# Kernel tuning notes

Hardware: AMD Instinct MI355X
Metric: run time of the kernel (lower is better)

## Reference

```python
import jax, jax.numpy as jnp
import numpy as np
import math

D = 2048  # hidden_size
B, S = 4, 2048
EPS = 1e-5


def _ln(z, g, b):
    m = jnp.mean(z, axis=-1, keepdims=True)
    v = jnp.mean(jnp.square(z - m), axis=-1, keepdims=True)
    return (z - m) * jax.lax.rsqrt(v + EPS) * g + b


def _rotate_half(x):
    h = x.shape[-1] // 2
    return jnp.concatenate([-x[..., h:], x[..., :h]], axis=-1)


def _mas_normalize(logits):
    m = jnp.max(jnp.abs(logits), axis=-1, keepdims=True)
    return logits / (m + 1e-9)


def setup_inputs() -> dict:
    key = jax.random.key(0)
    ks = jax.random.split(key, 12)
    std = 0.02
    return {
        "x": jax.random.normal(ks[0], (B, S, D), dtype=jnp.float32),
        "position_ids": jnp.arange(S, dtype=jnp.int32),
        "ln1_g": jnp.ones((D,), jnp.float32),
        "ln1_b": jnp.zeros((D,), jnp.float32),
        # stacked params for [q, k, v, o]
        "mu_w": std * jax.random.normal(ks[1], (4, D, D), dtype=jnp.float32),
        "mu_b": jnp.zeros((4, D), jnp.float32),
        "proto_w": std * jax.random.normal(ks[2], (4, D, D), dtype=jnp.float32),
        "gate": jnp.zeros((4, D), jnp.float32),
        "pt_w": std * jax.random.normal(ks[3], (4, D, D), dtype=jnp.float32),
        "pln_g": jnp.ones((4, D), jnp.float32),
        "pln_b": jnp.zeros((4, D), jnp.float32),
        "incoming": std * jax.random.normal(ks[4], (4, D, D), dtype=jnp.float32),
    }


def reference(x, position_ids, ln1_g, ln1_b, mu_w, mu_b, proto_w, gate,
              pt_w, pln_g, pln_b, incoming):
    d = x.shape[-1]
    inv_sqrt_d = 1.0 / math.sqrt(d)

    # proto_state = proto_weight + LN(Linear(incoming))  per module [4, D, D]
    prc = jnp.einsum('nij,noj->nio', incoming, pt_w)
    proto_state = proto_w + _ln(prc, pln_g[:, None, :], pln_b[:, None, :])

    ln1_out = _ln(x, ln1_g, ln1_b)            # [B,S,D]
    ctx = jnp.mean(ln1_out, axis=1)           # [B,D]

    # qkv computation outputs: silu(ln1_out @ mu_w.T + mu_b) for n in {q,k,v}
    comp = jax.nn.silu(jnp.einsum('bsd,nod->nbso', ln1_out, mu_w[:3])
                       + mu_b[:3][:, None, None, :])            # [3,B,S,D]
    # routing from context vector
    match_ctx = jnp.einsum('bd,nod->nbo', ctx, proto_state[:3]) * inv_sqrt_d
    routing = match_ctx + gate[:3][:, None, :]                  # [3,B,D]
    gating = _mas_normalize(routing)
    masked = gating[:, :, None, :] * comp                       # [3,B,S,D]
    q, k, v = masked[0], masked[1], masked[2]

    # RoPE over full hidden dim (num_heads == 1)
    seq = position_ids.shape[0]
    inv_freq = 1.0 / (10000.0 ** (jnp.arange(0, d, 2, dtype=jnp.float32) / d))
    t = jnp.arange(seq, dtype=jnp.float32)
    freqs = t[:, None] * inv_freq[None, :]
    emb = jnp.concatenate([freqs, freqs], axis=-1)              # [S,D]
    cos = jnp.cos(emb)[position_ids]
    sin = jnp.sin(emb)[position_ids]
    q = q * cos + _rotate_half(q) * sin
    k = k * cos + _rotate_half(k) * sin

    # causal single-head attention, scale 1/sqrt(head_dim=D)
    scores = jnp.einsum('bqd,bkd->bqk', q, k) * inv_sqrt_d      # [B,S,S]
    causal = jnp.tril(jnp.ones((seq, seq), dtype=bool))
    scores = jnp.where(causal, scores, jnp.finfo(scores.dtype).min)
    probs = jax.nn.softmax(scores, axis=-1)
    attn_out = jnp.einsum('bqk,bkd->bqd', probs, v)             # [B,S,D]

    # output SPL + routing
    ctx_o = jnp.mean(attn_out, axis=1)
    c_o = jax.nn.silu(jnp.einsum('bsd,od->bso', attn_out, mu_w[3]) + mu_b[3])
    match_o = jnp.einsum('bd,od->bo', ctx_o, proto_state[3]) * inv_sqrt_d
    gating_o = _mas_normalize(match_o + gate[3])
    x_out = x + gating_o[:, None, :] * c_o
    return x_out
```

## Files before the change

kernel.cpp:

```cpp
#include <hip/hip_runtime.h>
#include <hip/hip_bf16.h>
#include <hip/hip_fp16.h>

#define Dh 2048
#define Bh 4
#define Sh 2048
#define NROW 8192
#define HALF 1024
#define INV_SQRT_D 0.022097086912079608f
#define LNEPS 1e-5f

typedef __hip_bfloat16 bf16;
typedef short short8 __attribute__((ext_vector_type(8)));
typedef float f32x4 __attribute__((ext_vector_type(4)));
typedef unsigned short ushort8v __attribute__((ext_vector_type(8)));
typedef unsigned short ushort4v __attribute__((ext_vector_type(4)));

__device__ inline float h2f_bits(unsigned short u) {
  __half h;
  *(unsigned short*)&h = u;
  return __half2float(h);
}

__device__ inline float warp_sum(float x) {
#pragma unroll
  for (int o = 32; o > 0; o >>= 1) x += __shfl_down(x, o);
  return x;
}
__device__ inline float warp_max(float x) {
#pragma unroll
  for (int o = 32; o > 0; o >>= 1) x = fmaxf(x, __shfl_down(x, o));
  return x;
}
__device__ inline float block_sum(float x, float* sm4) {
  x = warp_sum(x);
  int w = threadIdx.x >> 6;
  if ((threadIdx.x & 63) == 0) sm4[w] = x;
  __syncthreads();
  float r = sm4[0] + sm4[1] + sm4[2] + sm4[3];
  __syncthreads();
  return r;
}
__device__ inline float block_max(float x, float* sm4) {
  x = warp_max(x);
  int w = threadIdx.x >> 6;
  if ((threadIdx.x & 63) == 0) sm4[w] = x;
  __syncthreads();
  float r = fmaxf(fmaxf(sm4[0], sm4[1]), fmaxf(sm4[2], sm4[3]));
  __syncthreads();
  return r;
}

__device__ inline void gload_lds16(const void* g, void* lds) {
  __builtin_amdgcn_global_load_lds(
      (const __attribute__((address_space(1))) unsigned int*)(unsigned long long)g,
      (__attribute__((address_space(3))) unsigned int*)(unsigned long long)lds,
      16, 0, 0);
}

#define MM4(R, AF, B0, B1, B2, B3)                                             \
  acc[R][0] = __builtin_amdgcn_mfma_f32_16x16x32_bf16(AF, B0, acc[R][0], 0, 0, 0); \
  acc[R][1] = __builtin_amdgcn_mfma_f32_16x16x32_bf16(AF, B1, acc[R][1], 0, 0, 0); \
  acc[R][2] = __builtin_amdgcn_mfma_f32_16x16x32_bf16(AF, B2, acc[R][2], 0, 0, 0); \
  acc[R][3] = __builtin_amdgcn_mfma_f32_16x16x32_bf16(AF, B3, acc[R][3], 0, 0, 0);

template <int MODE>
__global__ __launch_bounds__(512) void pgemm(
    const bf16* __restrict__ Aall, const bf16* __restrict__ Ball,
    void* __restrict__ Call, int N, int K, int lda, int ldb,
    long sAz, long sBz, long sCz,
    const float* __restrict__ e0, const float* __restrict__ e1,
    const float* __restrict__ e2) {
  const int bm0 = blockIdx.x * 256;
  const int bn0 = blockIdx.y * 256;
  if (MODE == 2 && bn0 > bm0 + 255) return;
  const int z = blockIdx.z;
  const bf16* A = Aall + (long)z * sAz;
  const bf16* B = Ball + (long)z * sBz;

  __shared__ __align__(16) char smem[131072];
  const int tid = threadIdx.x;
  const int l = tid & 63, w = tid >> 6;
  const int wr = w >> 2, wc = w & 3;

  f32x4 acc[8][4] = {};
  const int nt = K >> 6;

  const int sg = (((l & 7) ^ ((l >> 3) & 7)) << 3);
  const int srow = (w << 3) + (l >> 3);
  const bf16* aS0 = A + (long)(bm0 + srow) * lda + sg;
  const bf16* aS1 = A + (long)(bm0 + 64 + srow) * lda + sg;
  const bf16* aS2 = A + (long)(bm0 + 128 + srow) * lda + sg;
  const bf16* aS3 = A + (long)(bm0 + 192 + srow) * lda + sg;
  const bf16* bT0 = B + (long)(bn0 + srow) * ldb + sg;
  const bf16* bT1 = B + (long)(bn0 + 64 + srow) * ldb + sg;
  const bf16* bT2 = B + (long)(bn0 + 128 + srow) * ldb + sg;
  const bf16* bT3 = B + (long)(bn0 + 192 + srow) * ldb + sg;
  char* const dA = smem + (w << 10);
  char* const dB = smem + 65536 + (w << 10);

  auto stageA = [&](int tt) {
    int boff = (tt & 1) << 15;
    gload_lds16(aS0 + (tt << 6), dA + boff);
    gload_lds16(aS1 + (tt << 6), dA + boff + 8192);
    gload_lds16(aS2 + (tt << 6), dA + boff + 16384);
    gload_lds16(aS3 + (tt << 6), dA + boff + 24576);
  };
  auto stageB = [&](int tt) {
    int boff = (tt & 1) << 15;
    gload_lds16(bT0 + (tt << 6), dB + boff);
    gload_lds16(bT1 + (tt << 6), dB + boff + 8192);
    gload_lds16(bT2 + (tt << 6), dB + boff + 16384);
    gload_lds16(bT3 + (tt << 6), dB + boff + 24576);
  };

  stageA(0); stageB(0);
  if (nt > 1) stageB(1);
  if (nt > 1) asm volatile("s_waitcnt vmcnt(4)" ::: "memory");
  else        asm volatile("s_waitcnt vmcnt(0)" ::: "memory");
  __builtin_amdgcn_sched_barrier(0);
  asm volatile("s_barrier" ::: "memory");

  const int rslot = (((l >> 4) ^ (l & 7)) << 4);
  const int abyte = (((wr << 7) + (l & 15)) << 7) + rslot;
  const int bbyte = (((wc << 6) + (l & 15)) << 7) + rslot;

  for (int t = 0; t < nt; ++t) {
    const char* Ab = smem + ((t & 1) << 15);
    const char* Bb = smem + 65536 + ((t & 1) << 15);
    short8 b00 = *(const short8*)(Bb + bbyte);
    short8 b01 = *(const short8*)(Bb + bbyte + 2048);
    short8 b02 = *(const short8*)(Bb + bbyte + 4096);
    short8 b03 = *(const short8*)(Bb + bbyte + 6144);
    short8 b10 = *(const short8*)(Bb + (bbyte ^ 64));
    short8 b11 = *(const short8*)(Bb + ((bbyte + 2048) ^ 64));
    short8 b12 = *(const short8*)(Bb + ((bbyte + 4096) ^ 64));
    short8 b13 = *(const short8*)(Bb + ((bbyte + 6144) ^ 64));
    short8 a0 = *(const short8*)(Ab + abyte);
    short8 a1 = *(const short8*)(Ab + abyte + 2048);
    short8 a2 = *(const short8*)(Ab + abyte + 4096);
    short8 a3 = *(const short8*)(Ab + abyte + 6144);
    short8 a4 = *(const short8*)(Ab + abyte + 8192);
    short8 a5 = *(const short8*)(Ab + abyte + 10240);
    short8 a6 = *(const short8*)(Ab + abyte + 12288);
    short8 a7 = *(const short8*)(Ab + abyte + 14336);
    if (t + 1 < nt) stageA(t + 1);
    MM4(0, a0, b00, b01, b02, b03) MM4(1, a1, b00, b01, b02, b03)
    MM4(2, a2, b00, b01, b02, b03) MM4(3, a3, b00, b01, b02, b03)
    MM4(4, a4, b00, b01, b02, b03) MM4(5, a5, b00, b01, b02, b03)
    MM4(6, a6, b00, b01, b02, b03) MM4(7, a7, b00, b01, b02, b03)
    asm volatile("s_waitcnt lgkmcnt(0)" ::: "memory");
    asm volatile("s_barrier" ::: "memory");
    short8 c0 = *(const short8*)(Ab + (abyte ^ 64));
    short8 c1 = *(const short8*)(Ab + ((abyte + 2048) ^ 64));
    short8 c2 = *(const short8*)(Ab + ((abyte + 4096) ^ 64));
    short8 c3 = *(const short8*)(Ab + ((abyte + 6144) ^ 64));
    short8 c4 = *(const short8*)(Ab + ((abyte + 8192) ^ 64));
    short8 c5 = *(const short8*)(Ab + ((abyte + 10240) ^ 64));
    short8 c6 = *(const short8*)(Ab + ((abyte + 12288) ^ 64));
    short8 c7 = *(const short8*)(Ab + ((abyte + 14336) ^ 64));
    if (t + 2 < nt) stageB(t + 2);
    MM4(0, c0, b10, b11, b12, b13) MM4(1, c1, b10, b11, b12, b13)
    MM4(2, c2, b10, b11, b12, b13) MM4(3, c3, b10, b11, b12, b13)
    MM4(4, c4, b10, b11, b12, b13) MM4(5, c5, b10, b11, b12, b13)
    MM4(6, c6, b10, b11, b12, b13) MM4(7, c7, b10, b11, b12, b13)
    if (t < nt - 1) {
      asm volatile("s_waitcnt lgkmcnt(0)" ::: "memory");
      if (t + 2 < nt) asm volatile("s_waitcnt vmcnt(4)" ::: "memory");
      else            asm volatile("s_waitcnt vmcnt(0)" ::: "memory");
      __builtin_amdgcn_sched_barrier(0);
      asm volatile("s_barrier" ::: "memory");
    }
  }

  const int lc = l & 15, lr4 = (l >> 4) << 2;
#pragma unroll
  for (int fr = 0; fr < 8; ++fr) {
    int gr0 = bm0 + (wr << 7) + fr * 16 + lr4;
#pragma unroll
    for (int fc = 0; fc < 4; ++fc) {
      int gc = bn0 + (wc << 6) + fc * 16 + lc;
#pragma unroll
      for (int qv = 0; qv < 4; ++qv) {
        int gr = gr0 + qv;
        float a = acc[fr][fc][qv];
        if (MODE == 0) {
          ((float*)Call + (long)z * sCz)[(long)gr * N + gc] = a;
        } else if (MODE == 1) {
          float val = a + e0[z * Dh + gc];
          float sil = val / (1.f + __expf(-val));
          int bb = gr >> 11;
          float g = e1[(z * Bh + bb) * Dh + gc];
          ((bf16*)Call + (long)z * sCz)[(long)gr * N + gc] =
              __float2bfloat16(sil * g);
        } else if (MODE == 2) {
          ((__half*)Call + (long)z * sCz)[(long)gr * N + gc] =
              __float2half(a * INV_SQRT_D);
        } else {
          float val = a + e0[gc];
          float sil = val / (1.f + __expf(-val));
          int bb = gr >> 11;
          ((float*)Call)[(long)gr * N + gc] =
              e2[(long)gr * N + gc] + e1[bb * Dh + gc] * sil;
        }
      }
    }
  }
}

#define MM(R, AF)                                                              \
  acc[R][0] = __builtin_amdgcn_mfma_f32_16x16x32_bf16(AF, b0, acc[R][0], 0, 0, 0); \
  acc[R][1] = __builtin_amdgcn_mfma_f32_16x16x32_bf16(AF, b1, acc[R][1], 0, 0, 0); \
  acc[R][2] = __builtin_amdgcn_mfma_f32_16x16x32_bf16(AF, b2, acc[R][2], 0, 0, 0); \
  acc[R][3] = __builtin_amdgcn_mfma_f32_16x16x32_bf16(AF, b3, acc[R][3], 0, 0, 0);

__global__ __launch_bounds__(512) void pgemm_h(
    const bf16* __restrict__ Aall, const bf16* __restrict__ Ball,
    bf16* __restrict__ Call, int N, int lda, int ldb,
    long sAz, long sBz, long sCz) {
  const int fid = blockIdx.x;
  const int p = fid >> 8, q = fid & 255;
  const int mh = q >> 5;
  const int z = (q >> 3) & 3, ni = q & 7;
  const int mi = p ? (15 - mh) : mh;
  const int bm0 = mi * 128, bn0 = ni * 256;
  const bf16* A = Aall + (long)z * sAz;
  const bf16* B = Ball + (long)z * sBz;

  __shared__ __align__(16) char smem[49152];
  const int tid = threadIdx.x;
  const int l = tid & 63, w = tid >> 6;
  const int wr = w >> 2, wc = w & 3;
  f32x4 acc[4][4] = {};
  const int nt = (bm0 + 128) >> 5;

  const int sg = (((l & 3) ^ ((l >> 3) & 3)) << 3);
  const int srow = (w << 4) + (l >> 2);
  const bf16* aS  = A + (long)(bm0 + srow) * lda + sg;
  const bf16* bS0 = B + (long)(bn0 + srow) * ldb + sg;
  const bf16* bS1 = B + (long)(bn0 + 128 + srow) * ldb + sg;
  char* const dA = smem + (w << 10);
  char* const dB = smem + 8192 + (w << 10);

  auto stageA = [&](int tt) {
    gload_lds16(aS + (tt << 5), dA + (tt & 1) * 24576);
  };
  auto stageB = [&](int tt) {
    int boff = (tt & 1) * 24576;
    gload_lds16(bS0 + (tt << 5), dB + boff);
    gload_lds16(bS1 + (tt << 5), dB + boff + 8192);
  };

  stageA(0); stageB(0);
  if (nt > 1) stageB(1);
  if (nt > 1) asm volatile("s_waitcnt vmcnt(2)" ::: "memory");
  else        asm volatile("s_waitcnt vmcnt(0)" ::: "memory");
  __builtin_amdgcn_sched_barrier(0);
  asm volatile("s_barrier" ::: "memory");

  const int rslot = (((l >> 4) ^ ((l >> 1) & 3)) << 4);
  const int abyte = (((wr << 6) + (l & 15)) << 6) + rslot;
  const int bbyte = (((wc << 6) + (l & 15)) << 6) + rslot;

  for (int t = 0; t < nt; ++t) {
    const char* Ab = smem + (t & 1) * 24576;
    const char* Bb = Ab + 8192;
    short8 b0 = *(const short8*)(Bb + bbyte);
    short8 b1 = *(const short8*)(Bb + bbyte + 1024);
    short8 b2 = *(const short8*)(Bb + bbyte + 2048);
    short8 b3 = *(const short8*)(Bb + bbyte + 3072);
    short8 a0 = *(const short8*)(Ab + abyte);
    short8 a1 = *(const short8*)(Ab + abyte + 1024);
    if (t + 1 < nt) stageA(t + 1);
    MM(0, a0) MM(1, a1)
    asm volatile("s_waitcnt lgkmcnt(0)" ::: "memory");
    asm volatile("s_barrier" ::: "memory");
    short8 a2 = *(const short8*)(Ab + abyte + 2048);
    short8 a3 = *(const short8*)(Ab + abyte + 3072);
    if (t + 2 < nt) stageB(t + 2);
    MM(2, a2) MM(3, a3)
    if (t < nt - 1) {
      asm volatile("s_waitcnt lgkmcnt(0)" ::: "memory");
      if (t + 2 < nt) asm volatile("s_waitcnt vmcnt(2)" ::: "memory");
      else            asm volatile("s_waitcnt vmcnt(0)" ::: "memory");
      __builtin_amdgcn_sched_barrier(0);
      asm volatile("s_barrier" ::: "memory");
    }
  }

  const int lc = l & 15, lr4 = (l >> 4) << 2;
  bf16* C = Call + (long)z * sCz;
#pragma unroll
  for (int fr = 0; fr < 4; ++fr) {
    int gr0 = bm0 + (wr << 6) + fr * 16 + lr4;
#pragma unroll
    for (int fc = 0; fc < 4; ++fc) {
      int gc = bn0 + (wc << 6) + fc * 16 + lc;
#pragma unroll
      for (int qv = 0; qv < 4; ++qv)
        C[(long)(gr0 + qv) * N + gc] = __float2bfloat16(acc[fr][fc][qv]);
    }
  }
}

__global__ __launch_bounds__(256) void cvt3_kernel(
    const float* __restrict__ s0, const float* __restrict__ s1,
    const float* __restrict__ s2, bf16* __restrict__ o0, bf16* __restrict__ o1,
    bf16* __restrict__ o2, long n) {
  const float* in = (blockIdx.y == 0) ? s0 : (blockIdx.y == 1) ? s1 : s2;
  bf16* out = (blockIdx.y == 0) ? o0 : (blockIdx.y == 1) ? o1 : o2;
  long i = ((long)blockIdx.x * 256 + threadIdx.x) * 4;
  if (i >= n) return;
  float4 v = *(const float4*)(in + i);
  out[i + 0] = __float2bfloat16(v.x);
  out[i + 1] = __float2bfloat16(v.y);
  out[i + 2] = __float2bfloat16(v.z);
  out[i + 3] = __float2bfloat16(v.w);
}

__global__ __launch_bounds__(256) void transpose_kernel(const bf16* __restrict__ in,
                                                        bf16* __restrict__ out) {
  __shared__ bf16 t[64][65];
  int b = blockIdx.z;
  int s0 = blockIdx.x * 64, d0 = blockIdx.y * 64;
  const bf16* ib = in + (long)b * Sh * Dh;
  bf16* ob = out + (long)b * Sh * Dh;
  int tx = threadIdx.x & 63, ty = threadIdx.x >> 6;
#pragma unroll
  for (int r = ty; r < 64; r += 4) t[r][tx] = ib[(long)(s0 + r) * Dh + d0 + tx];
  __syncthreads();
#pragma unroll
  for (int r = ty; r < 64; r += 4) ob[(long)(d0 + r) * Sh + s0 + tx] = t[tx][r];
}

__global__ __launch_bounds__(256) void ln1_kernel(const float* __restrict__ x,
    const float* __restrict__ g, const float* __restrict__ b, bf16* __restrict__ out) {
  __shared__ float sm4[4];
  long r = blockIdx.x;
  const float* row = x + r * Dh;
  int i0 = threadIdx.x * 4, i1 = 1024 + threadIdx.x * 4;
  float4 v0 = *(const float4*)(row + i0);
  float4 v1 = *(const float4*)(row + i1);
  float s = v0.x + v0.y + v0.z + v0.w + v1.x + v1.y + v1.z + v1.w;
  float s2 = v0.x * v0.x + v0.y * v0.y + v0.z * v0.z + v0.w * v0.w +
             v1.x * v1.x + v1.y * v1.y + v1.z * v1.z + v1.w * v1.w;
  s = block_sum(s, sm4);
  s2 = block_sum(s2, sm4);
  float mean = s * (1.f / Dh);
  float rstd = rsqrtf(s2 * (1.f / Dh) - mean * mean + LNEPS);
  float4 g0 = *(const float4*)(g + i0);
  float4 g1 = *(const float4*)(g + i1);
  float4 b0 = *(const float4*)(b + i0);
  float4 b1 = *(const float4*)(b + i1);
  ushort4v u0, u1;
  {
    bf16 t0 = __float2bfloat16((v0.x - mean) * rstd * g0.x + b0.x);
    bf16 t1 = __float2bfloat16((v0.y - mean) * rstd * g0.y + b0.y);
    bf16 t2 = __float2bfloat16((v0.z - mean) * rstd * g0.z + b0.z);
    bf16 t3 = __float2bfloat16((v0.w - mean) * rstd * g0.w + b0.w);
    u0[0] = *(unsigned short*)&t0; u0[1] = *(unsigned short*)&t1;
    u0[2] = *(unsigned short*)&t2; u0[3] = *(unsigned short*)&t3;
    bf16 s0b = __float2bfloat16((v1.x - mean) * rstd * g1.x + b1.x);
    bf16 s1b = __float2bfloat16((v1.y - mean) * rstd * g1.y + b1.y);
    bf16 s2b = __float2bfloat16((v1.z - mean) * rstd * g1.z + b1.z);
    bf16 s3b = __float2bfloat16((v1.w - mean) * rstd * g1.w + b1.w);
    u1[0] = *(unsigned short*)&s0b; u1[1] = *(unsigned short*)&s1b;
    u1[2] = *(unsigned short*)&s2b; u1[3] = *(unsigned short*)&s3b;
  }
  *(ushort4v*)(out + r * Dh + i0) = u0;
  *(ushort4v*)(out + r * Dh + i1) = u1;
}

__global__ __launch_bounds__(256) void meanrow_kernel(const bf16* __restrict__ in,
                                                      float* __restrict__ outbd) {
  int gid = blockIdx.x * 256 + threadIdx.x;
  int s0 = blockIdx.y * 128;
  long base = ((long)(gid >> 11) * Sh + s0) * Dh + (gid & 2047);
  float s = 0.f;
  for (int t = 0; t < 128; ++t) s += __bfloat162float(in[base + (long)t * Dh]);
  atomicAdd(&outbd[gid], s * (1.f / Sh));
}

__global__ __launch_bounds__(256) void route_kernel(
    const float* __restrict__ prc, const float* __restrict__ proto_w,
    const float* __restrict__ pln_g, const float* __restrict__ pln_b,
    const float* __restrict__ gate, const float* __restrict__ ctx,
    float* __restrict__ routing, float* __restrict__ ps3) {
  __shared__ float sm4[4];
  int i = blockIdx.x, n = blockIdx.y;
  long rb = ((long)n * Dh + i) * Dh;
  float v[8];
  float s = 0.f, s2 = 0.f;
#pragma unroll
  for (int c = 0; c < 8; ++c) {
    float t = prc[rb + threadIdx.x + c * 256];
    v[c] = t; s += t; s2 += t * t;
  }
  s = block_sum(s, sm4);
  s2 = block_sum(s2, sm4);
  float mean = s * (1.f / Dh);
  float rstd = rsqrtf(s2 * (1.f / Dh) - mean * mean + LNEPS);
  if (n == 3) {
#pragma unroll
    for (int c = 0; c < 8; ++c) {
      int o = threadIdx.x + c * 256;
      float ps = proto_w[rb + o] + (v[c] - mean) * rstd * pln_g[3 * Dh + o] + pln_b[3 * Dh + o];
      ps3[(long)i * Dh + o] = ps;
    }
  } else {
    float acc[4] = {0.f, 0.f, 0.f, 0.f};
#pragma unroll
    for (int c = 0; c < 8; ++c) {
      int o = threadIdx.x + c * 256;
      float ps = proto_w[rb + o] + (v[c] - mean) * rstd * pln_g[n * Dh + o] + pln_b[n * Dh + o];
#pragma unroll
      for (int b = 0; b < 4; ++b) acc[b] += ps * ctx[b * Dh + o];
    }
    for (int b = 0; b < 4; ++b) {
      float r = block_sum(acc[b], sm4);
      if (threadIdx.x == 0)
        routing[(n * 4 + b) * Dh + i] = r * INV_SQRT_D + gate[n * Dh + i];
    }
  }
}

__global__ __launch_bounds__(256) void route_o_kernel(
    const float* __restrict__ ps3, const float* __restrict__ ctxo,
    const float* __restrict__ gate, float* __restrict__ routing) {
  __shared__ float sm4[4];
  int i = blockIdx.x;
  float acc[4] = {0.f, 0.f, 0.f, 0.f};
#pragma unroll
  for (int c = 0; c < 8; ++c) {
    int o = threadIdx.x + c * 256;
    float p = ps3[(long)i * Dh + o];
#pragma unroll
    for (int b = 0; b < 4; ++b) acc[b] += p * ctxo[b * Dh + o];
  }
  for (int b = 0; b < 4; ++b) {
    float r = block_sum(acc[b], sm4);
    if (threadIdx.x == 0)
      routing[(12 + b) * Dh + i] = r * INV_SQRT_D + gate[3 * Dh + i];
  }
}

__global__ __launch_bounds__(256) void masnorm_kernel(const float* __restrict__ rin,
                                                      float* __restrict__ gout) {
  __shared__ float sm4[4];
  long r = blockIdx.x;
  float m = 0.f;
#pragma unroll
  for (int c = 0; c < 8; ++c)
    m = fmaxf(m, fabsf(rin[r * Dh + threadIdx.x + c * 256]));
  m = block_max(m, sm4);
  float inv = 1.f / (m + 1e-9f);
#pragma unroll
  for (int c = 0; c < 8; ++c) {
    int o = threadIdx.x + c * 256;
    gout[r * Dh + o] = rin[r * Dh + o] * inv;
  }
}

__global__ __launch_bounds__(256) void rope_table_kernel(float* __restrict__ cosT,
                                                         float* __restrict__ sinT) {
  int idx = blockIdx.x * 256 + threadIdx.x;
  int t = idx >> 10, f = idx & 1023;
  float inv_freq = expf(-(float)f * (9.210340371976184f / 1024.f));
  float ang = (float)t * inv_freq;
  cosT[idx] = cosf(ang);
  sinT[idx] = sinf(ang);
}

__global__ __launch_bounds__(256) void rope_kernel(bf16* __restrict__ q, bf16* __restrict__ k,
    const int* __restrict__ pos, const float* __restrict__ cosT,
    const float* __restrict__ sinT) {
  long r = blockIdx.x;
  int s = (int)(r & (Sh - 1));
  int p = pos[s];
#pragma unroll
  for (int c = 0; c < 4; ++c) {
    int t = threadIdx.x + c * 256;
    float cv = cosT[(long)p * HALF + t];
    float sv = sinT[(long)p * HALF + t];
    long i1 = r * Dh + t, i2 = i1 + HALF;
    float q1 = __bfloat162float(q[i1]), q2 = __bfloat162float(q[i2]);
    q[i1] = __float2bfloat16(q1 * cv - q2 * sv);
    q[i2] = __float2bfloat16(q2 * cv + q1 * sv);
    float k1 = __bfloat162float(k[i1]), k2 = __bfloat162float(k[i2]);
    k[i1] = __float2bfloat16(k1 * cv - k2 * sv);
    k[i2] = __float2bfloat16(k2 * cv + k1 * sv);
  }
}

__global__ __launch_bounds__(256) void softmax_kernel(const unsigned short* __restrict__ scores,
                                                      bf16* __restrict__ probs) {
  __shared__ float buf[Sh];
  __shared__ float sm4[4];
  long r = blockIdx.x;
  int qi = (int)(r & (Sh - 1));
  const unsigned short* row = scores + r * (long)Sh;
  bf16* prow = probs + r * (long)Sh;
  int tid = threadIdx.x;
  int n = qi + 1, nv = n & ~7;
  float m = -3.0e38f;
  for (int o = tid * 8; o < nv; o += 2048) {
    ushort8v v = *(const ushort8v*)(row + o);
#pragma unroll
    for (int j = 0; j < 8; ++j) {
      float x = h2f_bits(v[j]);
      buf[o + j] = x;
      m = fmaxf(m, x);
    }
  }
  for (int o = nv + tid; o < n; o += 256) {
    float x = h2f_bits(row[o]); buf[o] = x; m = fmaxf(m, x);
  }
  m = block_max(m, sm4);
  float s = 0.f;
  for (int o = tid; o < n; o += 256) {
    float e = __expf(buf[o] - m); buf[o] = e; s += e;
  }
  s = block_sum(s, sm4);
  float inv = 1.f / s;
  for (int o = tid * 8; o < nv; o += 2048) {
    ushort8v u;
#pragma unroll
    for (int j = 0; j < 8; ++j) {
      bf16 t = __float2bfloat16(buf[o + j] * inv);
      u[j] = *(unsigned short*)&t;
    }
    *(ushort8v*)(prow + o) = u;
  }
  for (int o = nv + tid; o < n; o += 256) prow[o] = __float2bfloat16(buf[o] * inv);
  int za = (n + 7) & ~7;
  for (int o = n + tid; o < za && o < Sh; o += 256) prow[o] = __float2bfloat16(0.f);
  ushort8v zz = {0, 0, 0, 0, 0, 0, 0, 0};
  for (int o = za + tid * 8; o < Sh; o += 2048) *(ushort8v*)(prow + o) = zz;
}

extern "C" void kernel_launch(void* const* d_in, const int* in_sizes, int n_in,
                              void* d_out, int out_size, void* d_ws, size_t ws_size,
                              hipStream_t stream) {
  const float* x       = (const float*)d_in[0];
  const int*   pos     = (const int*)d_in[1];
  const float* ln1_g   = (const float*)d_in[2];
  const float* ln1_b   = (const float*)d_in[3];
  const float* mu_w    = (const float*)d_in[4];
  const float* mu_b    = (const float*)d_in[5];
  const float* proto_w = (const float*)d_in[6];
  const float* gate    = (const float*)d_in[7];
  const float* pt_w    = (const float*)d_in[8];
  const float* pln_g   = (const float*)d_in[9];
  const float* pln_b   = (const float*)d_in[10];
  const float* incoming= (const float*)d_in[11];

  char* w = (char*)d_ws;
  const long BF = 33554432L;
  bf16*  ln1    = (bf16*)(w);
  bf16*  qb     = (bf16*)(w + BF);
  bf16*  kb     = (bf16*)(w + 2 * BF);
  bf16*  vb     = (bf16*)(w + 3 * BF);
  bf16*  attn   = (bf16*)(w + 4 * BF);
  bf16*  mu_wb  = (bf16*)(w + 5 * BF);
  bf16*  ptw_b  = (bf16*)(w + 6 * BF);
  bf16*  vT     = ptw_b;
  bf16*  inc_b  = (bf16*)(w + 7 * BF);
  bf16*  probs  = inc_b;
  float* ps3    = (float*)(w + 8 * BF);
  float* cosT   = (float*)(w + 8 * BF + 16777216L);
  float* sinT   = cosT + (long)Sh * HALF;
  float* ctx    = sinT + (long)Sh * HALF;
  float* ctxo   = ctx + Bh * Dh;
  float* routing= ctxo + Bh * Dh;
  float* gating = routing + 16 * Dh;
  float*  prc    = (float*)d_out;
  __half* scores = (__half*)d_out;

  const long DD4 = 4L * Dh * Dh;

  hipMemsetAsync(ctx, 0, 2L * Bh * Dh * sizeof(float), stream);

  rope_table_kernel<<<(Sh * HALF) / 256, 256, 0, stream>>>(cosT, sinT);
  cvt3_kernel<<<dim3(DD4 / 1024, 3), 256, 0, stream>>>(
      mu_w, incoming, pt_w, mu_wb, inc_b, ptw_b, DD4);
  ln1_kernel<<<NROW, 256, 0, stream>>>(x, ln1_g, ln1_b, ln1);
  meanrow_kernel<<<dim3(32, 16), 256, 0, stream>>>(ln1, ctx);
  pgemm<0><<<dim3(8, 8, 4), 512, 0, stream>>>(
      inc_b, ptw_b, prc, Dh, Dh, Dh, Dh,
      (long)Dh * Dh, (long)Dh * Dh, (long)Dh * Dh, nullptr, nullptr, nullptr);
  route_kernel<<<dim3(Dh, 4), 256, 0, stream>>>(prc, proto_w, pln_g, pln_b,
                                                gate, ctx, routing, ps3);
  masnorm_kernel<<<12, 256, 0, stream>>>(routing, gating);
  pgemm<1><<<dim3(32, 8, 3), 512, 0, stream>>>(
      ln1, mu_wb, qb, Dh, Dh, Dh, Dh,
      0L, (long)Dh * Dh, (long)NROW * Dh, mu_b, gating, nullptr);
  rope_kernel<<<NROW, 256, 0, stream>>>(qb, kb, pos, cosT, sinT);
  pgemm<2><<<dim3(8, 8, 4), 512, 0, stream>>>(
      qb, kb, scores, Sh, Dh, Dh, Dh,
      (long)Sh * Dh, (long)Sh * Dh, (long)Sh * Sh, nullptr, nullptr, nullptr);
  softmax_kernel<<<Bh * Sh, 256, 0, stream>>>((const unsigned short*)scores, probs);
  transpose_kernel<<<dim3(32, 32, 4), 256, 0, stream>>>(vb, vT);
  pgemm_h<<<512, 512, 0, stream>>>(
      probs, vT, attn, Dh, Sh, Sh,
      (long)Sh * Sh, (long)Dh * Sh, (long)Sh * Dh);
  meanrow_kernel<<<dim3(32, 16), 256, 0, stream>>>(attn, ctxo);
  route_o_kernel<<<Dh, 256, 0, stream>>>(ps3, ctxo, gate, routing);
  masnorm_kernel<<<4, 256, 0, stream>>>(routing + 12 * Dh, gating + 12 * Dh);
  pgemm<4><<<dim3(32, 8, 1), 512, 0, stream>>>(
      attn, mu_wb + 3L * Dh * Dh, d_out, Dh, Dh, Dh, Dh,
      0L, 0L, 0L, mu_b + 3 * Dh, gating + 12 * Dh, x);
}
```

Measured before the change: 630.9 us.

## Switch GEMM to 32x32x16 MFMA with a fragment-native LDS layout

Replaces the 16x16x32 bf16 MFMA tiling with 32x32x16 instructions, so each wave holds a 4x2 grid of 32x32 accumulators. The global-to-LDS staging is rearranged so each wave writes 32-row slabs in the order the MFMA operands are read, and the XOR bank swizzle is dropped in favour of plain linear offsets. The aim is fewer MFMA issues and fewer LDS reads per k-step. The unswizzled layout may bring LDS bank conflicts, and the epilogue row/column mapping is rewritten to match the 32x32 output layout.

```diff
diff --git a/kernel.cpp b/kernel.cpp
--- a/kernel.cpp
+++ b/kernel.cpp
@@ -13,6 +13,7 @@
 typedef __hip_bfloat16 bf16;
 typedef short short8 __attribute__((ext_vector_type(8)));
 typedef float f32x4 __attribute__((ext_vector_type(4)));
+typedef float f32x16 __attribute__((ext_vector_type(16)));
 typedef unsigned short ushort8v __attribute__((ext_vector_type(8)));
 typedef unsigned short ushort4v __attribute__((ext_vector_type(4)));
 
@@ -58,11 +59,8 @@
       16, 0, 0);
 }
 
-#define MM4(R, AF, B0, B1, B2, B3)                                             \
-  acc[R][0] = __builtin_amdgcn_mfma_f32_16x16x32_bf16(AF, B0, acc[R][0], 0, 0, 0); \
-  acc[R][1] = __builtin_amdgcn_mfma_f32_16x16x32_bf16(AF, B1, acc[R][1], 0, 0, 0); \
-  acc[R][2] = __builtin_amdgcn_mfma_f32_16x16x32_bf16(AF, B2, acc[R][2], 0, 0, 0); \
-  acc[R][3] = __builtin_amdgcn_mfma_f32_16x16x32_bf16(AF, B3, acc[R][3], 0, 0, 0);
+#define MM32(RB, CB, AF, BF)                                                   \
+  acc[RB][CB] = __builtin_amdgcn_mfma_f32_32x32x16_bf16(AF, BF, acc[RB][CB], 0, 0, 0);
 
 template <int MODE>
 __global__ __launch_bounds__(512) void pgemm(
@@ -83,35 +81,30 @@
   const int l = tid & 63, w = tid >> 6;
   const int wr = w >> 2, wc = w & 3;
 
-  f32x4 acc[8][4] = {};
+  f32x16 acc[4][2] = {};
   const int nt = K >> 6;
 
-  const int sg = (((l & 7) ^ ((l >> 3) & 7)) << 3);
-  const int srow = (w << 3) + (l >> 3);
-  const bf16* aS0 = A + (long)(bm0 + srow) * lda + sg;
-  const bf16* aS1 = A + (long)(bm0 + 64 + srow) * lda + sg;
-  const bf16* aS2 = A + (long)(bm0 + 128 + srow) * lda + sg;
-  const bf16* aS3 = A + (long)(bm0 + 192 + srow) * lda + sg;
-  const bf16* bT0 = B + (long)(bn0 + srow) * ldb + sg;
-  const bf16* bT1 = B + (long)(bn0 + 64 + srow) * ldb + sg;
-  const bf16* bT2 = B + (long)(bn0 + 128 + srow) * ldb + sg;
-  const bf16* bT3 = B + (long)(bn0 + 192 + srow) * ldb + sg;
-  char* const dA = smem + (w << 10);
-  char* const dB = smem + 65536 + (w << 10);
+  const int lrow = l & 31, lkh = l >> 5;
+  const bf16* aS = A + (long)(bm0 + (w << 5) + lrow) * lda + (lkh << 3);
+  const bf16* bS = B + (long)(bn0 + (w << 5) + lrow) * ldb + (lkh << 3);
+  char* const dA = smem + (w << 12);
+  char* const dB = smem + 65536 + (w << 12);
 
   auto stageA = [&](int tt) {
     int boff = (tt & 1) << 15;
-    gload_lds16(aS0 + (tt << 6), dA + boff);
-    gload_lds16(aS1 + (tt << 6), dA + boff + 8192);
-    gload_lds16(aS2 + (tt << 6), dA + boff + 16384);
-    gload_lds16(aS3 + (tt << 6), dA + boff + 24576);
+    const bf16* s = aS + (tt << 6);
+    gload_lds16(s,      dA + boff);
+    gload_lds16(s + 16, dA + boff + 1024);
+    gload_lds16(s + 32, dA + boff + 2048);
+    gload_lds16(s + 48, dA + boff + 3072);
   };
   auto stageB = [&](int tt) {
     int boff = (tt & 1) << 15;
-    gload_lds16(bT0 + (tt << 6), dB + boff);
-    gload_lds16(bT1 + (tt << 6), dB + boff + 8192);
-    gload_lds16(bT2 + (tt << 6), dB + boff + 16384);
-    gload_lds16(bT3 + (tt << 6), dB + boff + 24576);
+    const bf16* s = bS + (tt << 6);
+    gload_lds16(s,      dB + boff);
+    gload_lds16(s + 16, dB + boff + 1024);
+    gload_lds16(s + 32, dB + boff + 2048);
+    gload_lds16(s + 48, dB + boff + 3072);
   };
 
   stageA(0); stageB(0);
@@ -121,49 +114,57 @@
   __builtin_amdgcn_sched_barrier(0);
   asm volatile("s_barrier" ::: "memory");
 
-  const int rslot = (((l >> 4) ^ (l & 7)) << 4);
-  const int abyte = (((wr << 7) + (l & 15)) << 7) + rslot;
-  const int bbyte = (((wc << 6) + (l & 15)) << 7) + rslot;
+  const int l16 = l << 4;
+  const int aBase = (wr << 14) + l16;
+  const int bBase = (wc << 13) + l16;
 
   for (int t = 0; t < nt; ++t) {
     const char* Ab = smem + ((t & 1) << 15);
     const char* Bb = smem + 65536 + ((t & 1) << 15);
-    short8 b00 = *(const short8*)(Bb + bbyte);
-    short8 b01 = *(const short8*)(Bb + bbyte + 2048);
-    short8 b02 = *(const short8*)(Bb + bbyte + 4096);
-    short8 b03 = *(const short8*)(Bb + bbyte + 6144);
-    short8 b10 = *(const short8*)(Bb + (bbyte ^ 64));
-    short8 b11 = *(const short8*)(Bb + ((bbyte + 2048) ^ 64));
-    short8 b12 = *(const short8*)(Bb + ((bbyte + 4096) ^ 64));
-    short8 b13 = *(const short8*)(Bb + ((bbyte + 6144) ^ 64));
-    short8 a0 = *(const short8*)(Ab + abyte);
-    short8 a1 = *(const short8*)(Ab + abyte + 2048);
-    short8 a2 = *(const short8*)(Ab + abyte + 4096);
-    short8 a3 = *(const short8*)(Ab + abyte + 6144);
-    short8 a4 = *(const short8*)(Ab + abyte + 8192);
-    short8 a5 = *(const short8*)(Ab + abyte + 10240);
-    short8 a6 = *(const short8*)(Ab + abyte + 12288);
-    short8 a7 = *(const short8*)(Ab + abyte + 14336);
+    short8 b00 = *(const short8*)(Bb + bBase);
+    short8 b01 = *(const short8*)(Bb + bBase + 1024);
+    short8 b02 = *(const short8*)(Bb + bBase + 2048);
+    short8 b03 = *(const short8*)(Bb + bBase + 3072);
+    short8 b10 = *(const short8*)(Bb + bBase + 4096);
+    short8 b11 = *(const short8*)(Bb + bBase + 5120);
+    short8 b12 = *(const short8*)(Bb + bBase + 6144);
+    short8 b13 = *(const short8*)(Bb + bBase + 7168);
+    short8 a00 = *(const short8*)(Ab + aBase);
+    short8 a01 = *(const short8*)(Ab + aBase + 1024);
+    short8 a02 = *(const short8*)(Ab + aBase + 2048);
+    short8 a03 = *(const short8*)(Ab + aBase + 3072);
+    short8 a10 = *(const short8*)(Ab + aBase + 4096);
+    short8 a11 = *(const short8*)(Ab + aBase + 5120);
+    short8 a12 = *(const short8*)(Ab + aBase + 6144);
+    short8 a13 = *(const short8*)(Ab + aBase + 7168);
     if (t + 1 < nt) stageA(t + 1);
-    MM4(0, a0, b00, b01, b02, b03) MM4(1, a1, b00, b01, b02, b03)
-    MM4(2, a2, b00, b01, b02, b03) MM4(3, a3, b00, b01, b02, b03)
-    MM4(4, a4, b00, b01, b02, b03) MM4(5, a5, b00, b01, b02, b03)
-    MM4(6, a6, b00, b01, b02, b03) MM4(7, a7, b00, b01, b02, b03)
+    MM32(0, 0, a00, b00) MM32(0, 1, a00, b10)
+    MM32(1, 0, a10, b00) MM32(1, 1, a10, b10)
+    MM32(0, 0, a01, b01) MM32(0, 1, a01, b11)
+    MM32(1, 0, a11, b01) MM32(1, 1, a11, b11)
+    MM32(0, 0, a02, b02) MM32(0, 1, a02, b12)
+    MM32(1, 0, a12, b02) MM32(1, 1, a12, b12)
+    MM32(0, 0, a03, b03) MM32(0, 1, a03, b13)
+    MM32(1, 0, a13, b03) MM32(1, 1, a13, b13)
     asm volatile("s_waitcnt lgkmcnt(0)" ::: "memory");
     asm volatile("s_barrier" ::: "memory");
-    short8 c0 = *(const short8*)(Ab + (abyte ^ 64));
-    short8 c1 = *(const short8*)(Ab + ((abyte + 2048) ^ 64));
-    short8 c2 = *(const short8*)(Ab + ((abyte + 4096) ^ 64));
-    short8 c3 = *(const short8*)(Ab + ((abyte + 6144) ^ 64));
-    short8 c4 = *(const short8*)(Ab + ((abyte + 8192) ^ 64));
-    short8 c5 = *(const short8*)(Ab + ((abyte + 10240) ^ 64));
-    short8 c6 = *(const short8*)(Ab + ((abyte + 12288) ^ 64));
-    short8 c7 = *(const short8*)(Ab + ((abyte + 14336) ^ 64));
+    short8 a20 = *(const short8*)(Ab + aBase + 8192);
+    short8 a21 = *(const short8*)(Ab + aBase + 9216);
+    short8 a22 = *(const short8*)(Ab + aBase + 10240);
+    short8 a23 = *(const short8*)(Ab + aBase + 11264);
+    short8 a30 = *(const short8*)(Ab + aBase + 12288);
+    short8 a31 = *(const short8*)(Ab + aBase + 13312);
+    short8 a32 = *(const short8*)(Ab + aBase + 14336);
+    short8 a33 = *(const short8*)(Ab + aBase + 15360);
     if (t + 2 < nt) stageB(t + 2);
-    MM4(0, c0, b10, b11, b12, b13) MM4(1, c1, b10, b11, b12, b13)
-    MM4(2, c2, b10, b11, b12, b13) MM4(3, c3, b10, b11, b12, b13)
-    MM4(4, c4, b10, b11, b12, b13) MM4(5, c5, b10, b11, b12, b13)
-    MM4(6, c6, b10, b11, b12, b13) MM4(7, c7, b10, b11, b12, b13)
+    MM32(2, 0, a20, b00) MM32(2, 1, a20, b10)
+    MM32(3, 0, a30, b00) MM32(3, 1, a30, b10)
+    MM32(2, 0, a21, b01) MM32(2, 1, a21, b11)
+    MM32(3, 0, a31, b01) MM32(3, 1, a31, b11)
+    MM32(2, 0, a22, b02) MM32(2, 1, a22, b12)
+    MM32(3, 0, a32, b02) MM32(3, 1, a32, b12)
+    MM32(2, 0, a23, b03) MM32(2, 1, a23, b13)
+    MM32(3, 0, a33, b03) MM32(3, 1, a33, b13)
     if (t < nt - 1) {
       asm volatile("s_waitcnt lgkmcnt(0)" ::: "memory");
       if (t + 2 < nt) asm volatile("s_waitcnt vmcnt(4)" ::: "memory");
@@ -173,17 +174,16 @@
     }
   }
 
-  const int lc = l & 15, lr4 = (l >> 4) << 2;
-#pragma unroll
-  for (int fr = 0; fr < 8; ++fr) {
-    int gr0 = bm0 + (wr << 7) + fr * 16 + lr4;
-#pragma unroll
-    for (int fc = 0; fc < 4; ++fc) {
-      int gc = bn0 + (wc << 6) + fc * 16 + lc;
-#pragma unroll
-      for (int qv = 0; qv < 4; ++qv) {
-        int gr = gr0 + qv;
-        float a = acc[fr][fc][qv];
+  const int lc = l & 31, lh4 = (l >> 5) << 2;
+#pragma unroll
+  for (int rb = 0; rb < 4; ++rb) {
+#pragma unroll
+    for (int cb = 0; cb < 2; ++cb) {
+      int gc = bn0 + (wc << 6) + cb * 32 + lc;
+#pragma unroll
+      for (int reg = 0; reg < 16; ++reg) {
+        int gr = bm0 + (wr << 7) + rb * 32 + (reg & 3) + ((reg >> 2) << 3) + lh4;
+        float a = acc[rb][cb][reg];
         if (MODE == 0) {
           ((float*)Call + (long)z * sCz)[(long)gr * N + gc] = a;
         } else if (MODE == 1) {
```

Result: slower. 722.3 us (+14.5%).
